# Kernel tuning notes

Measured on AMD Instinct MI355X. Metric: run time of the kernel, lower is better.

Reference implementation:

```python
import jax, jax.numpy as jnp
import numpy as np

H = 768       # hidden_size
HEADS = 8     # num_heads
T = 3         # num_timesteps
B = 128       # molecules in batch
N_ATOM = 48   # atoms per molecule
E_INTRA = 96  # intra-molecule directed edges per molecule
NPG = N_ATOM + 1          # nodes per graph (incl. virtual)
EPG = E_INTRA + N_ATOM    # edges per graph (incl. atom->virtual)
N = B * NPG
E = B * EPG


def setup_inputs() -> dict:
    key = jax.random.key(0)
    ks = jax.random.split(key, 10)
    atom_feat = jax.random.normal(ks[0], (B, N_ATOM, H), dtype=jnp.float32)
    mol_feat = jax.random.normal(ks[1], (B, H), dtype=jnp.float32)
    # node features with virtual node (=mol_feat) appended per graph, as in add_virtual_nodes_and_edges
    h_nodes = jnp.concatenate([atom_feat, mol_feat[:, None, :]], axis=1).reshape(N, H)
    off = jnp.arange(B, dtype=jnp.int32) * NPG
    intra_src = jax.random.randint(ks[2], (B, E_INTRA), 0, N_ATOM, dtype=jnp.int32) + off[:, None]
    intra_dst = jax.random.randint(ks[3], (B, E_INTRA), 0, N_ATOM, dtype=jnp.int32) + off[:, None]
    virt_src = jnp.arange(N_ATOM, dtype=jnp.int32)[None, :] + off[:, None]
    virt_dst = jnp.broadcast_to((off + N_ATOM)[:, None], (B, N_ATOM))
    src = jnp.concatenate([intra_src, virt_src], axis=1).reshape(E)
    dst = jnp.concatenate([intra_dst, virt_dst], axis=1).reshape(E)
    virtual_nids = off + N_ATOM  # last node of each graph (cumsum(batch_num_nodes)-1)
    attn_eids = ((jnp.arange(B, dtype=jnp.int32) * EPG)[:, None]
                 + E_INTRA + jnp.arange(N_ATOM, dtype=jnp.int32)[None, :]).reshape(-1)
    s = 0.02
    W_src = jax.random.normal(ks[4], (T, H, HEADS * H), dtype=jnp.float32) * s
    W_dst = jax.random.normal(ks[5], (T, H, HEADS * H), dtype=jnp.float32) * s
    attn_a = jax.random.normal(ks[6], (T, HEADS, H), dtype=jnp.float32) * s
    W_ih = jax.random.normal(ks[7], (T, 3 * H, H), dtype=jnp.float32) * s
    W_hh = jax.random.normal(ks[8], (T, 3 * H, H), dtype=jnp.float32) * s
    b_src = jnp.zeros((T, HEADS * H), jnp.float32)
    b_dst = jnp.zeros((T, HEADS * H), jnp.float32)
    b_ih = jnp.zeros((T, 3 * H), jnp.float32)
    b_hh = jnp.zeros((T, 3 * H), jnp.float32)
    return {"h_nodes": h_nodes, "mol_feat": mol_feat, "W_src": W_src, "b_src": b_src,
            "W_dst": W_dst, "b_dst": b_dst, "attn_a": attn_a, "W_ih": W_ih, "W_hh": W_hh,
            "b_ih": b_ih, "b_hh": b_hh, "src": src, "dst": dst,
            "virtual_nids": virtual_nids, "attn_eids": attn_eids}


def _gru_cell(x, hprev, W_ih_t, W_hh_t, b_ih_t, b_hh_t):
    # torch.nn.GRUCell: gates ordered r, z, n
    gi = x @ W_ih_t.T + b_ih_t
    gh = hprev @ W_hh_t.T + b_hh_t
    ir, iz, inn = jnp.split(gi, 3, axis=-1)
    hr, hz, hn = jnp.split(gh, 3, axis=-1)
    r = jax.nn.sigmoid(ir + hr)
    z = jax.nn.sigmoid(iz + hz)
    n = jnp.tanh(inn + r * hn)
    return (1.0 - z) * n + z * hprev


def _forward(h_nodes, mol_feat, W_src, b_src, W_dst, b_dst, attn_a,
             W_ih, W_hh, b_ih, b_hh, src, dst, virtual_nids, attn_eids):
    h = h_nodes
    mol_emb = mol_feat
    attns = []
    for t in range(T):
        # GATv2Conv (DGL, eval mode so feat_drop/attn_drop are identity)
        fs = (h @ W_src[t] + b_src[t]).reshape(N, HEADS, H)
        fd = (h @ W_dst[t] + b_dst[t]).reshape(N, HEADS, H)
        e = jax.nn.leaky_relu(fs[src] + fd[dst], negative_slope=0.2)  # [E, heads, H]
        logits = jnp.einsum('ehd,hd->eh', e, attn_a[t])               # [E, heads]
        # edge softmax over incoming edges per destination node
        m = jax.ops.segment_max(logits, dst, num_segments=N)
        ex = jnp.exp(logits - m[dst])
        ssum = jax.ops.segment_sum(ex, dst, num_segments=N)
        a = ex / ssum[dst]                                            # [E, heads]
        rst = jax.ops.segment_sum(a[:, :, None] * fs[src], dst, num_segments=N)  # [N, heads, H]
        h = rst.mean(axis=1)                                          # mean over heads
        out_virtual = h[virtual_nids]                                 # [B, H]
        mol_emb = jax.nn.relu(_gru_cell(out_virtual, mol_emb, W_ih[t], W_hh[t], b_ih[t], b_hh[t]))
        attns.append(a.mean(axis=1)[attn_eids])                       # attention on virtual edges
    return mol_emb, jnp.stack(attns)


def reference(h_nodes, mol_feat, W_src, b_src, W_dst, b_dst, attn_a,
              W_ih, W_hh, b_ih, b_hh, src, dst, virtual_nids, attn_eids):
    return _forward(h_nodes, mol_feat, W_src, b_src, W_dst, b_dst, attn_a,
                    W_ih, W_hh, b_ih, b_hh, src, dst, virtual_nids, attn_eids)
```

## Files before the change

### kernel.cpp

```cpp
#include <hip/hip_runtime.h>
#include <hip/hip_bf16.h>

typedef __hip_bfloat16 bf16;
typedef float f32x4 __attribute__((ext_vector_type(4)));
typedef __bf16 bf16x8 __attribute__((ext_vector_type(8)));
typedef short s16x8 __attribute__((ext_vector_type(8)));
typedef short s16x2 __attribute__((ext_vector_type(2)));

#define HDIM 768
#define NHEAD 8
#define BMOL 128
#define NPG 49
#define EPG 144
#define NNODE (BMOL * NPG)
#define NEDGE (BMOL * EPG)
#define NH 6144
#define G3 2304

__device__ __forceinline__ float b2f(short s) {
    unsigned int u = ((unsigned int)(unsigned short)s) << 16;
    return __builtin_bit_cast(float, u);
}

__device__ __forceinline__ void async16(const bf16* g, bf16* l) {
    __builtin_amdgcn_global_load_lds(
        (const __attribute__((address_space(1))) void*)g,
        (__attribute__((address_space(3))) void*)l, 16, 0, 0);
}

#define VMCNT(n) asm volatile("s_waitcnt vmcnt(" #n ")" ::: "memory")
#define SBAR()                                 \
    do {                                       \
        asm volatile("" ::: "memory");         \
        __builtin_amdgcn_s_barrier();          \
        asm volatile("" ::: "memory");         \
    } while (0)

__global__ __launch_bounds__(512, 2) void gemm_bt8(
    const bf16* __restrict__ A, const bf16* __restrict__ Bt0,
    const bf16* __restrict__ Bt1, const float* __restrict__ bias0,
    const float* __restrict__ bias1, bf16* __restrict__ C0,
    bf16* __restrict__ C1) {
    __shared__ __align__(16) char smem[131072];
    bf16* lA = (bf16*)smem;
    bf16* lB = (bf16*)(smem + 65536);

    const int tid = threadIdx.x;
    const int lane = tid & 63;
    const int wave = tid >> 6;
    const int l16 = lane & 15;
    const int quad = lane >> 4;
    const int wm = wave >> 2;
    const int wn = wave & 3;
    const int K = HDIM;

    int id = blockIdx.y * 24 + blockIdx.x;
    const int xcd = id & 7;
    const int loc = id >> 3;
    const int mc = loc / 15;
    const int rem = loc % 15;
    const int ncol = rem / 5;
    const int moff = rem % 5;
    const int m0 = (mc * 5 + moff) * 256;
    const int n0 = (xcd * 3 + ncol) * 256;

    const bf16* Bt = blockIdx.z ? Bt1 : Bt0;
    const float* bias = blockIdx.z ? bias1 : bias0;
    bf16* C = blockIdx.z ? C1 : C0;

    const int srow = tid >> 3;
    const int ecol =
        ((tid & 7) * 8) ^ ((srow & 1) * 32) ^ ((srow & 2) * 8);
    const bf16* gAr[4];
#pragma unroll
    for (int hc = 0; hc < 4; ++hc) {
        int r = m0 + srow + hc * 64;
        if (r > NNODE - 1) r = NNODE - 1;
        gAr[hc] = A + (size_t)r * K + ecol;
    }
    const bf16* gB = Bt + (size_t)(n0 + srow) * K + ecol;
    const size_t hstep = (size_t)128 * K;
    const size_t cstep = (size_t)64 * K;
    bf16* dA = lA + tid * 8;
    bf16* dB = lB + tid * 8;

#define STAGE_A(buf, h, kt)                                     \
    do {                                                        \
        bf16* _d = dA + (buf)*16384 + (h)*8192;                 \
        async16(gAr[(h)*2] + (size_t)(kt) * 64, _d);            \
        async16(gAr[(h)*2 + 1] + (size_t)(kt) * 64, _d + 4096); \
    } while (0)
#define STAGE_B(buf, h, kt)                                     \
    do {                                                        \
        const bf16* _s = gB + (h)*hstep + (size_t)(kt) * 64;    \
        bf16* _d = dB + (buf)*16384 + (h)*8192;                 \
        async16(_s, _d);                                        \
        async16(_s + cstep, _d + 4096);                         \
    } while (0)

    const int q16 = quad * 16;
    const int sw = ((l16 & 1) << 6) | ((l16 & 2) << 4);
    const char* laRow = (const char*)lA + wm * 16384 + l16 * 128;
    const char* lbRow =
        (const char*)lB + (wn >> 1) * 16384 + (wn & 1) * 8192 + l16 * 128;

#define LDA8(buf, f, ks) \
    (*(const bf16x8*)(laRow + (buf)*32768 + (f)*2048 + ((q16 + (ks)*64) ^ sw)))
#define LDB8(buf, j, ks) \
    (*(const bf16x8*)(lbRow + (buf)*32768 + (j)*2048 + ((q16 + (ks)*64) ^ sw)))

    f32x4 acc[8][4];
#pragma unroll
    for (int i = 0; i < 8; ++i)
#pragma unroll
        for (int j = 0; j < 4; ++j) acc[i][j] = (f32x4){0.f, 0.f, 0.f, 0.f};
    bf16x8 bfr[4][2];

#define MF(i, j, ks, areg)                                             \
    acc[i][j] = __builtin_amdgcn_mfma_f32_16x16x32_bf16(areg, bfr[j][ks], \
                                                        acc[i][j], 0, 0, 0)

#define PHASE(buf, q, LB, STG, WAIT)                                   \
    do {                                                               \
        bf16x8 a00 = LDA8(buf, (q)*2, 0);                              \
        bf16x8 a01 = LDA8(buf, (q)*2, 1);                              \
        bf16x8 a10 = LDA8(buf, (q)*2 + 1, 0);                          \
        bf16x8 a11 = LDA8(buf, (q)*2 + 1, 1);                          \
        if (LB) {                                                      \
            bfr[0][0] = LDB8(buf, 0, 0); bfr[0][1] = LDB8(buf, 0, 1);  \
            bfr[1][0] = LDB8(buf, 1, 0); bfr[1][1] = LDB8(buf, 1, 1);  \
            bfr[2][0] = LDB8(buf, 2, 0); bfr[2][1] = LDB8(buf, 2, 1);  \
            bfr[3][0] = LDB8(buf, 3, 0); bfr[3][1] = LDB8(buf, 3, 1);  \
        }                                                              \
        STG;                                                           \
        SBAR();                                                        \
        __builtin_amdgcn_s_setprio(1);                                 \
        MF((q)*2, 0, 0, a00); MF((q)*2, 1, 0, a00);                    \
        MF((q)*2, 2, 0, a00); MF((q)*2, 3, 0, a00);                    \
        MF((q)*2 + 1, 0, 0, a10); MF((q)*2 + 1, 1, 0, a10);            \
        MF((q)*2 + 1, 2, 0, a10); MF((q)*2 + 1, 3, 0, a10);            \
        MF((q)*2, 0, 1, a01); MF((q)*2, 1, 1, a01);                    \
        MF((q)*2, 2, 1, a01); MF((q)*2, 3, 1, a01);                    \
        MF((q)*2 + 1, 0, 1, a11); MF((q)*2 + 1, 1, 1, a11);            \
        MF((q)*2 + 1, 2, 1, a11); MF((q)*2 + 1, 3, 1, a11);            \
        __builtin_amdgcn_s_setprio(0);                                 \
        WAIT;                                                          \
        SBAR();                                                        \
    } while (0)

    STAGE_A(0, 0, 0); STAGE_A(0, 1, 0);
    STAGE_B(0, 0, 0); STAGE_B(0, 1, 0);
    STAGE_B(1, 0, 1); STAGE_B(1, 1, 1);
    VMCNT(4);
    SBAR();

    int t0 = 0;
    for (int it = 0; it < 5; ++it, t0 += 2) {
        PHASE(0, 0, 1, STAGE_A(1, 0, t0 + 1), );
        PHASE(0, 1, 0, STAGE_A(1, 1, t0 + 1), );
        PHASE(0, 2, 0, STAGE_B(0, 0, t0 + 2), );
        PHASE(0, 3, 0, STAGE_B(0, 1, t0 + 2), VMCNT(4));
        PHASE(1, 0, 1, STAGE_A(0, 0, t0 + 2), );
        PHASE(1, 1, 0, STAGE_A(0, 1, t0 + 2), );
        PHASE(1, 2, 0, STAGE_B(1, 0, t0 + 3), );
        PHASE(1, 3, 0, STAGE_B(1, 1, t0 + 3), VMCNT(4));
    }
    PHASE(0, 0, 1, STAGE_A(1, 0, 11), );
    PHASE(0, 1, 0, STAGE_A(1, 1, 11), );
    PHASE(0, 2, 0, , );
    PHASE(0, 3, 0, , VMCNT(0));
    PHASE(1, 0, 1, , );
    PHASE(1, 1, 0, , );
    PHASE(1, 2, 0, , );
    PHASE(1, 3, 0, , );

    __syncthreads();
#pragma unroll
    for (int i = 0; i < 8; ++i) {
        const int rloc = wm * 128 + i * 16 + quad * 4;
#pragma unroll
        for (int j = 0; j < 4; ++j) {
            const int cloc = wn * 64 + j * 16 + l16;
            const float bc = bias[n0 + cloc];
#pragma unroll
            for (int r = 0; r < 4; ++r) {
                const int rr = rloc + r;
                int off = (rr * 512 + cloc * 2) ^ ((rr & 4) ? 32 : 0);
                *(bf16*)(smem + off) = __float2bfloat16(acc[i][j][r] + bc);
            }
        }
    }
    __syncthreads();
#pragma unroll
    for (int k = 0; k < 16; ++k) {
        const int off = (k * 512 + tid) * 16;
        const int row = off >> 9;
        const int bcol = (off & 511) ^ ((row & 4) ? 32 : 0);
        if (m0 + row < NNODE) {
            bf16x8 v = *(const bf16x8*)(smem + off);
            *(bf16x8*)(C + (size_t)(m0 + row) * NH + n0 + (bcol >> 1)) = v;
        }
    }
#undef PHASE
#undef MF
#undef LDA8
#undef LDB8
#undef STAGE_A
#undef STAGE_B
}

__global__ __launch_bounds__(256) void gemm_small(
    const bf16* __restrict__ hws, const int* __restrict__ vnids,
    const bf16* __restrict__ A1, const bf16* __restrict__ B0,
    const bf16* __restrict__ B1, const float* __restrict__ bias0,
    const float* __restrict__ bias1, float* __restrict__ C0,
    float* __restrict__ C1, const bf16* __restrict__ A0) {
    __shared__ __align__(16) bf16 lA[32 * 32];
    __shared__ __align__(16) bf16 lB[256 * 32];
    const int tid = threadIdx.x;
    const int lane = tid & 63;
    const int wave = tid >> 6;
    const int l16 = lane & 15;
    const int quad = lane >> 4;
    const int K = HDIM;
    const int y0 = blockIdx.y * 32;
    const int x0 = blockIdx.x * 256;
    const bf16* Bt = blockIdx.z ? B1 : B0;
    const float* bias = blockIdx.z ? bias1 : bias0;
    float* C = blockIdx.z ? C1 : C0;

    const int ry = y0 + (tid >> 2);
    const bf16* gA;
    if (blockIdx.z)
        gA = A1 + (size_t)ry * K + (tid & 3) * 8;
    else if (A0)
        gA = A0 + (size_t)(ry & 127) * K + (tid & 3) * 8;
    else
        gA = hws + (size_t)vnids[ry & 127] * K + (tid & 3) * 8;
    const bf16* gB = Bt + (size_t)(x0 + (tid >> 2)) * K + (tid & 3) * 8;
    bf16* lAp = lA + tid * 8;
    bf16* lBp = lB + tid * 8;
    const size_t rstep = (size_t)64 * K;

    f32x4 acc[2][4];
#pragma unroll
    for (int i = 0; i < 2; ++i)
#pragma unroll
        for (int j = 0; j < 4; ++j) acc[i][j] = (f32x4){0.f, 0.f, 0.f, 0.f};

    for (int k0 = 0; k0 < K; k0 += 32) {
        __syncthreads();
        if (tid < 128) async16(gA + k0, lAp);
        async16(gB + k0, lBp);
        async16(gB + k0 + rstep, lBp + 2048);
        async16(gB + k0 + 2 * rstep, lBp + 4096);
        async16(gB + k0 + 3 * rstep, lBp + 6144);
        __syncthreads();
        bf16x8 af[2], bfr[4];
#pragma unroll
        for (int i = 0; i < 2; ++i)
            af[i] = *(const bf16x8*)(lA + (i * 16 + l16) * 32 + quad * 8);
#pragma unroll
        for (int j = 0; j < 4; ++j)
            bfr[j] = *(const bf16x8*)(lB + (wave * 64 + j * 16 + l16) * 32 +
                                      quad * 8);
#pragma unroll
        for (int i = 0; i < 2; ++i)
#pragma unroll
            for (int j = 0; j < 4; ++j)
                acc[i][j] = __builtin_amdgcn_mfma_f32_16x16x32_bf16(
                    af[i], bfr[j], acc[i][j], 0, 0, 0);
    }

#pragma unroll
    for (int i = 0; i < 2; ++i) {
#pragma unroll
        for (int j = 0; j < 4; ++j) {
            int row = y0 + i * 16 + quad * 4;
            int col = x0 + wave * 64 + j * 16 + l16;
            float bc = bias[col];
#pragma unroll
            for (int r = 0; r < 4; ++r)
                C[(size_t)(row + r) * G3 + col] = acc[i][j][r] + bc;
        }
    }
}

__global__ __launch_bounds__(256) void gemm_gather_bt(
    const bf16* __restrict__ hws, const int* __restrict__ vnids,
    const bf16* __restrict__ Bt, const float* __restrict__ bias,
    bf16* __restrict__ C) {
    __shared__ __align__(16) bf16 lA[32 * 32];
    __shared__ __align__(16) bf16 lB[256 * 32];
    const int tid = threadIdx.x;
    const int lane = tid & 63;
    const int wave = tid >> 6;
    const int l16 = lane & 15;
    const int quad = lane >> 4;
    const int K = HDIM;
    const int y0 = blockIdx.y * 32;
    const int x0 = blockIdx.x * 256;

    const int ry = y0 + (tid >> 2);
    const bf16* gA = hws + (size_t)vnids[ry & 127] * K + (tid & 3) * 8;
    const bf16* gB = Bt + (size_t)(x0 + (tid >> 2)) * K + (tid & 3) * 8;
    bf16* lAp = lA + tid * 8;
    bf16* lBp = lB + tid * 8;
    const size_t rstep = (size_t)64 * K;

    f32x4 acc[2][4];
#pragma unroll
    for (int i = 0; i < 2; ++i)
#pragma unroll
        for (int j = 0; j < 4; ++j) acc[i][j] = (f32x4){0.f, 0.f, 0.f, 0.f};

    for (int k0 = 0; k0 < K; k0 += 32) {
        __syncthreads();
        if (tid < 128) async16(gA + k0, lAp);
        async16(gB + k0, lBp);
        async16(gB + k0 + rstep, lBp + 2048);
        async16(gB + k0 + 2 * rstep, lBp + 4096);
        async16(gB + k0 + 3 * rstep, lBp + 6144);
        __syncthreads();
        bf16x8 af[2], bfr[4];
#pragma unroll
        for (int i = 0; i < 2; ++i)
            af[i] = *(const bf16x8*)(lA + (i * 16 + l16) * 32 + quad * 8);
#pragma unroll
        for (int j = 0; j < 4; ++j)
            bfr[j] = *(const bf16x8*)(lB + (wave * 64 + j * 16 + l16) * 32 +
                                      quad * 8);
#pragma unroll
        for (int i = 0; i < 2; ++i)
#pragma unroll
            for (int j = 0; j < 4; ++j)
                acc[i][j] = __builtin_amdgcn_mfma_f32_16x16x32_bf16(
                    af[i], bfr[j], acc[i][j], 0, 0, 0);
    }

#pragma unroll
    for (int i = 0; i < 2; ++i) {
#pragma unroll
        for (int j = 0; j < 4; ++j) {
            int row = y0 + i * 16 + quad * 4;
            int col = x0 + wave * 64 + j * 16 + l16;
            float bc = bias[col];
#pragma unroll
            for (int r = 0; r < 4; ++r)
                C[(size_t)(row + r) * NH + col] =
                    __float2bfloat16(acc[i][j][r] + bc);
        }
    }
}

__global__ __launch_bounds__(256) void transpose_w(
    const float* __restrict__ W, bf16* __restrict__ Wt, int K, int Nn) {
    __shared__ bf16 tile[64][65];
    const int z = blockIdx.z;
    const float* Wp = W + (size_t)z * K * Nn;
    bf16* Wtp = Wt + (size_t)z * K * Nn;
    const int n0 = blockIdx.x * 64;
    const int k0 = blockIdx.y * 64;
    const int tx = threadIdx.x & 63;
    const int ty = threadIdx.x >> 6;
#pragma unroll
    for (int i = 0; i < 64; i += 4)
        tile[ty + i][tx] = __float2bfloat16(Wp[(size_t)(k0 + ty + i) * Nn + n0 + tx]);
    __syncthreads();
#pragma unroll
    for (int i = 0; i < 64; i += 4)
        Wtp[(size_t)(n0 + ty + i) * K + k0 + tx] = tile[tx][ty + i];
}

__global__ void cvt_kernel(const float* __restrict__ x, bf16* __restrict__ y,
                           int n) {
    int i = blockIdx.x * 256 + threadIdx.x;
    if (i < n) y[i] = __float2bfloat16(x[i]);
}

__global__ __launch_bounds__(256) void logits_kernel(
    const bf16* __restrict__ fs, const bf16* __restrict__ fd,
    const float* __restrict__ attn_a_t, const int* __restrict__ src,
    const int* __restrict__ dst, float* __restrict__ logits) {
    __shared__ __align__(16) float s_a[NH];
    const int tid = threadIdx.x;
    for (int p = tid; p < NH; p += 256) s_a[p] = attn_a_t[p];
    __syncthreads();

    const int wave = tid >> 6;
    const int lane = tid & 63;
    const int e = blockIdx.x * 4 + wave;
    const int gs = src[e], gd = dst[e];
    const bf16* ps = fs + (size_t)gs * NH;
    const bf16* pd = fd + (size_t)gd * NH;
    const int h = lane >> 3;
    const int s = lane & 7;
    const int base = h * HDIM + s * 8;

    float acc = 0.f;
#pragma unroll
    for (int j = 0; j < 12; ++j) {
        const int off = base + j * 64;
        s16x8 a8 = *(const s16x8*)(ps + off);
        s16x8 d8 = *(const s16x8*)(pd + off);
        f32x4 av0 = *(const f32x4*)(s_a + off);
        f32x4 av1 = *(const f32x4*)(s_a + off + 4);
#pragma unroll
        for (int u = 0; u < 4; ++u) {
            float x = b2f(a8[u]) + b2f(d8[u]);
            x = (x > 0.f) ? x : 0.2f * x;
            acc += x * av0[u];
        }
#pragma unroll
        for (int u = 0; u < 4; ++u) {
            float x = b2f(a8[4 + u]) + b2f(d8[4 + u]);
            x = (x > 0.f) ? x : 0.2f * x;
            acc += x * av1[u];
        }
    }
    acc += __shfl_xor(acc, 1);
    acc += __shfl_xor(acc, 2);
    acc += __shfl_xor(acc, 4);
    if (s == 0) logits[(size_t)e * NHEAD + h] = acc;
}

__global__ __launch_bounds__(256) void logits_virt_kernel(
    const bf16* __restrict__ fs, const bf16* __restrict__ fdv,
    const float* __restrict__ attn_a_t, float* __restrict__ lgv) {
    __shared__ __align__(16) float s_a[NH];
    const int tid = threadIdx.x;
    for (int p = tid; p < NH; p += 256) s_a[p] = attn_a_t[p];
    __syncthreads();

    const int wave = tid >> 6;
    const int lane = tid & 63;
    const int e = blockIdx.x * 4 + wave;
    const int b = e / 48;
    const int i = e - b * 48;
    const bf16* ps = fs + (size_t)(b * NPG + i) * NH;
    const bf16* pd = fdv + (size_t)b * NH;
    const int h = lane >> 3;
    const int s = lane & 7;
    const int base = h * HDIM + s * 8;

    float acc = 0.f;
#pragma unroll
    for (int j = 0; j < 12; ++j) {
        const int off = base + j * 64;
        s16x8 a8 = *(const s16x8*)(ps + off);
        s16x8 d8 = *(const s16x8*)(pd + off);
        f32x4 av0 = *(const f32x4*)(s_a + off);
        f32x4 av1 = *(const f32x4*)(s_a + off + 4);
#pragma unroll
        for (int u = 0; u < 4; ++u) {
            float x = b2f(a8[u]) + b2f(d8[u]);
            x = (x > 0.f) ? x : 0.2f * x;
            acc += x * av0[u];
        }
#pragma unroll
        for (int u = 0; u < 4; ++u) {
            float x = b2f(a8[4 + u]) + b2f(d8[4 + u]);
            x = (x > 0.f) ? x : 0.2f * x;
            acc += x * av1[u];
        }
    }
    acc += __shfl_xor(acc, 1);
    acc += __shfl_xor(acc, 2);
    acc += __shfl_xor(acc, 4);
    if (s == 0) lgv[(size_t)e * NHEAD + h] = acc;
}

__global__ __launch_bounds__(256) void softmax_kernel(
    const float* __restrict__ logits, const int* __restrict__ dst,
    float* __restrict__ w, float* __restrict__ outv) {
    __shared__ float s_logit[EPG * NHEAD];
    __shared__ float s_w[EPG * NHEAD];
    __shared__ int s_ld[EPG];
    __shared__ float s_m[NPG * NHEAD], s_inv[NPG * NHEAD];
    const int tid = threadIdx.x;
    const int b = blockIdx.x;
    for (int p = tid; p < EPG * NHEAD; p += 256)
        s_logit[p] = logits[(size_t)b * EPG * NHEAD + p];
    if (tid < EPG) s_ld[tid] = dst[b * EPG + tid] - b * NPG;
    __syncthreads();

    for (int p = tid; p < NPG * NHEAD; p += 256) {
        int n = p >> 3, h = p & 7;
        float m = -3.0e38f;
        for (int le = 0; le < EPG; ++le)
            if (s_ld[le] == n) m = fmaxf(m, s_logit[le * NHEAD + h]);
        float ss = 0.f;
        for (int le = 0; le < EPG; ++le)
            if (s_ld[le] == n) ss += __expf(s_logit[le * NHEAD + h] - m);
        s_m[p] = m;
        s_inv[p] = (ss > 0.f) ? 1.f / ss : 0.f;
    }
    __syncthreads();

    for (int p = tid; p < EPG * NHEAD; p += 256) {
        int le = p >> 3, h = p & 7;
        int ld = s_ld[le];
        float a =
            0.125f * __expf(s_logit[p] - s_m[ld * NHEAD + h]) * s_inv[ld * NHEAD + h];
        s_w[p] = a;
        w[(size_t)b * EPG * NHEAD + p] = a;
    }
    __syncthreads();
    if (tid < 48) {
        float s = 0.f;
#pragma unroll
        for (int h = 0; h < NHEAD; ++h) s += s_w[(96 + tid) * NHEAD + h];
        outv[b * 48 + tid] = s;
    }
}

__global__ __launch_bounds__(64) void softmax_virt_kernel(
    const float* __restrict__ lgv, float* __restrict__ wv,
    float* __restrict__ outv) {
    __shared__ float s_w[48 * NHEAD];
    const int b = blockIdx.x;
    const int tid = threadIdx.x;
    if (tid < NHEAD) {
        const int h = tid;
        float m = -3.0e38f;
        for (int i = 0; i < 48; ++i)
            m = fmaxf(m, lgv[(size_t)(b * 48 + i) * NHEAD + h]);
        float ss = 0.f;
        for (int i = 0; i < 48; ++i)
            ss += __expf(lgv[(size_t)(b * 48 + i) * NHEAD + h] - m);
        float inv = (ss > 0.f) ? 1.f / ss : 0.f;
        for (int i = 0; i < 48; ++i) {
            float a =
                0.125f * __expf(lgv[(size_t)(b * 48 + i) * NHEAD + h] - m) * inv;
            s_w[i * NHEAD + h] = a;
            wv[(size_t)(b * 48 + i) * NHEAD + h] = a;
        }
    }
    __syncthreads();
    if (tid < 48) {
        float s = 0.f;
#pragma unroll
        for (int h = 0; h < NHEAD; ++h) s += s_w[tid * NHEAD + h];
        outv[b * 48 + tid] = s;
    }
}

__global__ __launch_bounds__(256) void aggregate_kernel(
    const bf16* __restrict__ fs, const float* __restrict__ w,
    const int* __restrict__ src, const int* __restrict__ dst,
    bf16* __restrict__ hout) {
    __shared__ float acc[NPG * 128];
    __shared__ float s_w[EPG * NHEAD];
    __shared__ int s_gs[EPG], s_ld[EPG];
    const int tid = threadIdx.x;
    const int c = blockIdx.x;
    const int b = blockIdx.y;
    const int grp = tid >> 6;
    const int l = tid & 63;
    if (tid < EPG) {
        int e = b * EPG + tid;
        s_gs[tid] = src[e];
        s_ld[tid] = dst[e] - b * NPG;
    }
    for (int p = tid; p < EPG * NHEAD; p += 256)
        s_w[p] = w[(size_t)b * EPG * NHEAD + p];
    for (int p = tid; p < NPG * 128; p += 256) acc[p] = 0.f;
    __syncthreads();

    const int dim = c * 128 + l * 2;
    for (int le4 = 0; le4 < EPG; le4 += 4) {
        const int le = le4 + grp;
        const bf16* p = fs + (size_t)s_gs[le] * NH + dim;
        float sum0 = 0.f, sum1 = 0.f;
#pragma unroll
        for (int h = 0; h < NHEAD; ++h) {
            s16x2 v = *(const s16x2*)(p + h * HDIM);
            float wv = s_w[le * NHEAD + h];
            sum0 += wv * b2f(v[0]);
            sum1 += wv * b2f(v[1]);
        }
        float* ap = &acc[s_ld[le] * 128 + l * 2];
        atomicAdd(ap, sum0);
        atomicAdd(ap + 1, sum1);
    }
    __syncthreads();
    for (int p = tid; p < NPG * 128; p += 256) {
        int n = p >> 7, d = p & 127;
        hout[((size_t)b * NPG + n) * HDIM + c * 128 + d] =
            __float2bfloat16(acc[p]);
    }
}

__global__ __launch_bounds__(256) void aggregate_virt_kernel(
    const bf16* __restrict__ fs, const float* __restrict__ wv,
    bf16* __restrict__ hv) {
    __shared__ float acc[128];
    __shared__ float s_w[48 * NHEAD];
    const int tid = threadIdx.x;
    const int c = blockIdx.x;
    const int b = blockIdx.y;
    const int grp = tid >> 6;
    const int l = tid & 63;
    for (int p = tid; p < 48 * NHEAD; p += 256)
        s_w[p] = wv[(size_t)b * 48 * NHEAD + p];
    if (tid < 128) acc[tid] = 0.f;
    __syncthreads();

    const int dim = c * 128 + l * 2;
    float sum0 = 0.f, sum1 = 0.f;
    for (int le = grp; le < 48; le += 4) {
        const bf16* p = fs + (size_t)(b * NPG + le) * NH + dim;
#pragma unroll
        for (int h = 0; h < NHEAD; ++h) {
            s16x2 v = *(const s16x2*)(p + h * HDIM);
            float w_ = s_w[le * NHEAD + h];
            sum0 += w_ * b2f(v[0]);
            sum1 += w_ * b2f(v[1]);
        }
    }
    atomicAdd(&acc[l * 2], sum0);
    atomicAdd(&acc[l * 2 + 1], sum1);
    __syncthreads();
    if (tid < 128)
        hv[(size_t)b * HDIM + c * 128 + tid] = __float2bfloat16(acc[tid]);
}

__global__ void init_memb_kernel(const float* __restrict__ mf,
                                 float* __restrict__ m32,
                                 bf16* __restrict__ m16) {
    int idx = blockIdx.x * 256 + threadIdx.x;
    float f = mf[idx];
    m32[idx] = f;
    m16[idx] = __float2bfloat16(f);
}

__global__ void gru_gate_kernel(const float* __restrict__ gi,
                                const float* __restrict__ gh,
                                float* __restrict__ m32, bf16* __restrict__ m16,
                                float* __restrict__ outp, int last) {
    int idx = blockIdx.x * 256 + threadIdx.x;
    int b = idx / HDIM, d = idx - b * HDIM;
    const float* gib = gi + (size_t)b * G3;
    const float* ghb = gh + (size_t)b * G3;
    float ir = gib[d], iz = gib[HDIM + d], in_ = gib[2 * HDIM + d];
    float hr = ghb[d], hz = ghb[HDIM + d], hn = ghb[2 * HDIM + d];
    float r = 1.f / (1.f + __expf(-(ir + hr)));
    float z = 1.f / (1.f + __expf(-(iz + hz)));
    float n = tanhf(in_ + r * hn);
    float hprev = m32[idx];
    float hnew = (1.f - z) * n + z * hprev;
    hnew = fmaxf(hnew, 0.f);
    m32[idx] = hnew;
    m16[idx] = __float2bfloat16(hnew);
    if (last) outp[idx] = hnew;
}

extern "C" void kernel_launch(void* const* d_in, const int* in_sizes, int n_in,
                              void* d_out, int out_size, void* d_ws,
                              size_t ws_size, hipStream_t stream) {
    const float* h_nodes = (const float*)d_in[0];
    const float* mol_feat = (const float*)d_in[1];
    const float* W_src = (const float*)d_in[2];
    const float* b_src = (const float*)d_in[3];
    const float* W_dst = (const float*)d_in[4];
    const float* b_dst = (const float*)d_in[5];
    const float* attn_a = (const float*)d_in[6];
    const float* W_ih = (const float*)d_in[7];
    const float* W_hh = (const float*)d_in[8];
    const float* b_ih = (const float*)d_in[9];
    const float* b_hh = (const float*)d_in[10];
    const int* src = (const int*)d_in[11];
    const int* dst = (const int*)d_in[12];
    const int* vnids = (const int*)d_in[13];
    float* out = (float*)d_out;

    char* p = (char*)d_ws;
    auto alloc = [&](size_t bytes) {
        char* r = p;
        p += (bytes + 255) & ~(size_t)255;
        return r;
    };
    bf16* wsrcT = (bf16*)alloc((size_t)3 * NH * HDIM * 2);
    bf16* wdstT = (bf16*)alloc((size_t)3 * NH * HDIM * 2);
    bf16* wihB = (bf16*)alloc((size_t)3 * G3 * HDIM * 2);
    bf16* whhB = (bf16*)alloc((size_t)3 * G3 * HDIM * 2);
    bf16* fs = (bf16*)alloc((size_t)NNODE * NH * 2);
    bf16* fd = (bf16*)alloc((size_t)NNODE * NH * 2);
    bf16* h_ws = (bf16*)alloc((size_t)NNODE * HDIM * 2);
    float* lg = (float*)alloc((size_t)NEDGE * NHEAD * 4);
    float* w_e = (float*)alloc((size_t)NEDGE * NHEAD * 4);
    float* memb32 = (float*)alloc((size_t)BMOL * HDIM * 4);
    bf16* memb16 = (bf16*)alloc((size_t)BMOL * HDIM * 2);
    float* gi = (float*)alloc((size_t)BMOL * G3 * 4);
    float* gh = (float*)alloc((size_t)BMOL * G3 * 4);

    dim3 tgrid(NH / 64, HDIM / 64, 3);
    transpose_w<<<tgrid, 256, 0, stream>>>(W_src, wsrcT, HDIM, NH);
    transpose_w<<<tgrid, 256, 0, stream>>>(W_dst, wdstT, HDIM, NH);
    {
        int n = 3 * G3 * HDIM;
        cvt_kernel<<<(n + 255) / 256, 256, 0, stream>>>(W_ih, wihB, n);
        cvt_kernel<<<(n + 255) / 256, 256, 0, stream>>>(W_hh, whhB, n);
    }
    {
        int n = NNODE * HDIM;
        cvt_kernel<<<(n + 255) / 256, 256, 0, stream>>>(h_nodes, h_ws, n);
    }
    init_memb_kernel<<<BMOL * HDIM / 256, 256, 0, stream>>>(mol_feat, memb32,
                                                            memb16);

    for (int t = 0; t < 3; ++t) {
        if (t < 2) {
            gemm_bt8<<<dim3(24, 25, 2), 512, 0, stream>>>(
                h_ws, wsrcT + (size_t)t * NH * HDIM,
                wdstT + (size_t)t * NH * HDIM, b_src + (size_t)t * NH,
                b_dst + (size_t)t * NH, fs, fd);
            logits_kernel<<<NEDGE / 4, 256, 0, stream>>>(
                fs, fd, attn_a + (size_t)t * NHEAD * HDIM, src, dst, lg);
            softmax_kernel<<<BMOL, 256, 0, stream>>>(
                lg, dst, w_e, out + BMOL * HDIM + t * BMOL * 48);
            aggregate_kernel<<<dim3(6, BMOL), 256, 0, stream>>>(fs, w_e, src,
                                                                dst, h_ws);
            gemm_small<<<dim3(G3 / 256, 4, 2), 256, 0, stream>>>(
                h_ws, vnids, memb16, wihB + (size_t)t * G3 * HDIM,
                whhB + (size_t)t * G3 * HDIM, b_ih + (size_t)t * G3,
                b_hh + (size_t)t * G3, gi, gh, (const bf16*)nullptr);
            gru_gate_kernel<<<BMOL * HDIM / 256, 256, 0, stream>>>(
                gi, gh, memb32, memb16, out, 0);
        } else {
            gemm_bt8<<<dim3(24, 25, 1), 512, 0, stream>>>(
                h_ws, wsrcT + (size_t)t * NH * HDIM,
                wdstT + (size_t)t * NH * HDIM, b_src + (size_t)t * NH,
                b_dst + (size_t)t * NH, fs, fd);
            gemm_gather_bt<<<dim3(NH / 256, 4), 256, 0, stream>>>(
                h_ws, vnids, wdstT + (size_t)t * NH * HDIM,
                b_dst + (size_t)t * NH, fd);
            logits_virt_kernel<<<(BMOL * 48) / 4, 256, 0, stream>>>(
                fs, fd, attn_a + (size_t)t * NHEAD * HDIM, lg);
            softmax_virt_kernel<<<BMOL, 64, 0, stream>>>(
                lg, w_e, out + BMOL * HDIM + t * BMOL * 48);
            aggregate_virt_kernel<<<dim3(6, BMOL), 256, 0, stream>>>(
                fs, w_e, h_ws);
            gemm_small<<<dim3(G3 / 256, 4, 2), 256, 0, stream>>>(
                h_ws, vnids, memb16, wihB + (size_t)t * G3 * HDIM,
                whhB + (size_t)t * G3 * HDIM, b_ih + (size_t)t * G3,
                b_hh + (size_t)t * G3, gi, gh, h_ws);
            gru_gate_kernel<<<BMOL * HDIM / 256, 256, 0, stream>>>(
                gi, gh, memb32, memb16, out, 1);
        }
    }
}
```

Measured before the change: 1.045 ms.

## Merge setup conversion kernels, fuse virtual logits+softmax, widen aggregate and logits work per block

Combines the two weight transposes into one launch and the four fp32-to-bf16 conversion kernels into a single cvt_all kernel. For the last timestep, virtual-edge logits and softmax are fused into one per-molecule kernel that keeps logits in shared memory. Each logits block now handles 16 edges instead of 4, and each aggregate block covers 256 dims using 4-wide loads instead of 128 dims with 2-wide loads. Together these cut launch count and global round trips, at the cost of fewer blocks (less parallelism) in logits, aggregate and virtual attention.

```diff
diff --git a/kernel.cpp b/kernel.cpp
--- a/kernel.cpp
+++ b/kernel.cpp
@@ -5,7 +5,7 @@
 typedef float f32x4 __attribute__((ext_vector_type(4)));
 typedef __bf16 bf16x8 __attribute__((ext_vector_type(8)));
 typedef short s16x8 __attribute__((ext_vector_type(8)));
-typedef short s16x2 __attribute__((ext_vector_type(2)));
+typedef short s16x4 __attribute__((ext_vector_type(4)));
 
 #define HDIM 768
 #define NHEAD 8
@@ -353,12 +353,15 @@
     }
 }
 
-__global__ __launch_bounds__(256) void transpose_w(
-    const float* __restrict__ W, bf16* __restrict__ Wt, int K, int Nn) {
+__global__ __launch_bounds__(256) void transpose_w2(
+    const float* __restrict__ Wa, bf16* __restrict__ WaT,
+    const float* __restrict__ Wb, bf16* __restrict__ WbT, int K, int Nn) {
     __shared__ bf16 tile[64][65];
     const int z = blockIdx.z;
-    const float* Wp = W + (size_t)z * K * Nn;
-    bf16* Wtp = Wt + (size_t)z * K * Nn;
+    const float* Wp = (z < 3 ? Wa + (size_t)z * K * Nn
+                             : Wb + (size_t)(z - 3) * K * Nn);
+    bf16* Wtp = (z < 3 ? WaT + (size_t)z * K * Nn
+                       : WbT + (size_t)(z - 3) * K * Nn);
     const int n0 = blockIdx.x * 64;
     const int k0 = blockIdx.y * 64;
     const int tx = threadIdx.x & 63;
@@ -372,10 +375,31 @@
         Wtp[(size_t)(n0 + ty + i) * K + k0 + tx] = tile[tx][ty + i];
 }
 
-__global__ void cvt_kernel(const float* __restrict__ x, bf16* __restrict__ y,
-                           int n) {
+__global__ void cvt_all(const float* __restrict__ W_ih,
+                        const float* __restrict__ W_hh, bf16* __restrict__ wihB,
+                        bf16* __restrict__ whhB,
+                        const float* __restrict__ h_nodes,
+                        bf16* __restrict__ h_ws, const float* __restrict__ mf,
+                        float* __restrict__ m32, bf16* __restrict__ m16) {
+    const int N1 = 3 * G3 * HDIM;
+    const int N2 = N1 + 3 * G3 * HDIM;
+    const int N3 = N2 + NNODE * HDIM;
+    const int N4 = N3 + BMOL * HDIM;
     int i = blockIdx.x * 256 + threadIdx.x;
-    if (i < n) y[i] = __float2bfloat16(x[i]);
+    if (i < N1) {
+        wihB[i] = __float2bfloat16(W_ih[i]);
+    } else if (i < N2) {
+        int k = i - N1;
+        whhB[k] = __float2bfloat16(W_hh[k]);
+    } else if (i < N3) {
+        int k = i - N2;
+        h_ws[k] = __float2bfloat16(h_nodes[k]);
+    } else if (i < N4) {
+        int k = i - N3;
+        float f = mf[k];
+        m32[k] = f;
+        m16[k] = __float2bfloat16(f);
+    }
 }
 
 __global__ __launch_bounds__(256) void logits_kernel(
@@ -389,85 +413,44 @@
 
     const int wave = tid >> 6;
     const int lane = tid & 63;
-    const int e = blockIdx.x * 4 + wave;
-    const int gs = src[e], gd = dst[e];
-    const bf16* ps = fs + (size_t)gs * NH;
-    const bf16* pd = fd + (size_t)gd * NH;
     const int h = lane >> 3;
     const int s = lane & 7;
     const int base = h * HDIM + s * 8;
-
-    float acc = 0.f;
-#pragma unroll
-    for (int j = 0; j < 12; ++j) {
-        const int off = base + j * 64;
-        s16x8 a8 = *(const s16x8*)(ps + off);
-        s16x8 d8 = *(const s16x8*)(pd + off);
-        f32x4 av0 = *(const f32x4*)(s_a + off);
-        f32x4 av1 = *(const f32x4*)(s_a + off + 4);
-#pragma unroll
-        for (int u = 0; u < 4; ++u) {
-            float x = b2f(a8[u]) + b2f(d8[u]);
-            x = (x > 0.f) ? x : 0.2f * x;
-            acc += x * av0[u];
-        }
-#pragma unroll
-        for (int u = 0; u < 4; ++u) {
-            float x = b2f(a8[4 + u]) + b2f(d8[4 + u]);
-            x = (x > 0.f) ? x : 0.2f * x;
-            acc += x * av1[u];
-        }
-    }
-    acc += __shfl_xor(acc, 1);
-    acc += __shfl_xor(acc, 2);
-    acc += __shfl_xor(acc, 4);
-    if (s == 0) logits[(size_t)e * NHEAD + h] = acc;
-}
-
-__global__ __launch_bounds__(256) void logits_virt_kernel(
-    const bf16* __restrict__ fs, const bf16* __restrict__ fdv,
-    const float* __restrict__ attn_a_t, float* __restrict__ lgv) {
-    __shared__ __align__(16) float s_a[NH];
-    const int tid = threadIdx.x;
-    for (int p = tid; p < NH; p += 256) s_a[p] = attn_a_t[p];
-    __syncthreads();
-
-    const int wave = tid >> 6;
-    const int lane = tid & 63;
-    const int e = blockIdx.x * 4 + wave;
-    const int b = e / 48;
-    const int i = e - b * 48;
-    const bf16* ps = fs + (size_t)(b * NPG + i) * NH;
-    const bf16* pd = fdv + (size_t)b * NH;
-    const int h = lane >> 3;
-    const int s = lane & 7;
-    const int base = h * HDIM + s * 8;
-
-    float acc = 0.f;
-#pragma unroll
-    for (int j = 0; j < 12; ++j) {
-        const int off = base + j * 64;
-        s16x8 a8 = *(const s16x8*)(ps + off);
-        s16x8 d8 = *(const s16x8*)(pd + off);
-        f32x4 av0 = *(const f32x4*)(s_a + off);
-        f32x4 av1 = *(const f32x4*)(s_a + off + 4);
-#pragma unroll
-        for (int u = 0; u < 4; ++u) {
-            float x = b2f(a8[u]) + b2f(d8[u]);
-            x = (x > 0.f) ? x : 0.2f * x;
-            acc += x * av0[u];
-        }
-#pragma unroll
-        for (int u = 0; u < 4; ++u) {
-            float x = b2f(a8[4 + u]) + b2f(d8[4 + u]);
-            x = (x > 0.f) ? x : 0.2f * x;
-            acc += x * av1[u];
-        }
-    }
-    acc += __shfl_xor(acc, 1);
-    acc += __shfl_xor(acc, 2);
-    acc += __shfl_xor(acc, 4);
-    if (s == 0) lgv[(size_t)e * NHEAD + h] = acc;
+    const int e0 = blockIdx.x * 16 + wave * 4;
+
+#pragma unroll
+    for (int ee = 0; ee < 4; ++ee) {
+        const int e = e0 + ee;
+        const int gs = src[e], gd = dst[e];
+        const bf16* ps = fs + (size_t)gs * NH;
+        const bf16* pd = fd + (size_t)gd * NH;
+
+        float acc = 0.f;
+#pragma unroll
+        for (int j = 0; j < 12; ++j) {
+            const int off = base + j * 64;
+            s16x8 a8 = *(const s16x8*)(ps + off);
+            s16x8 d8 = *(const s16x8*)(pd + off);
+            f32x4 av0 = *(const f32x4*)(s_a + off);
+            f32x4 av1 = *(const f32x4*)(s_a + off + 4);
+#pragma unroll
+            for (int u = 0; u < 4; ++u) {
+                float x = b2f(a8[u]) + b2f(d8[u]);
+                x = (x > 0.f) ? x : 0.2f * x;
+                acc += x * av0[u];
+            }
+#pragma unroll
+            for (int u = 0; u < 4; ++u) {
+                float x = b2f(a8[4 + u]) + b2f(d8[4 + u]);
+                x = (x > 0.f) ? x : 0.2f * x;
+                acc += x * av1[u];
+            }
+        }
+        acc += __shfl_xor(acc, 1);
+        acc += __shfl_xor(acc, 2);
+        acc += __shfl_xor(acc, 4);
+        if (s == 0) logits[(size_t)e * NHEAD + h] = acc;
+    }
 }
 
 __global__ __launch_bounds__(256) void softmax_kernel(
@@ -514,34 +497,74 @@
     }
 }
 
-__global__ __launch_bounds__(64) void softmax_virt_kernel(
-    const float* __restrict__ lgv, float* __restrict__ wv,
+__global__ __launch_bounds__(256) void attn_virt_kernel(
+    const bf16* __restrict__ fs, const bf16* __restrict__ fdv,
+    const float* __restrict__ attn_a_t, float* __restrict__ wv,
     float* __restrict__ outv) {
+    __shared__ __align__(16) float s_a[NH];
+    __shared__ float s_lg[48 * NHEAD];
     __shared__ float s_w[48 * NHEAD];
+    const int tid = threadIdx.x;
     const int b = blockIdx.x;
-    const int tid = threadIdx.x;
+    for (int p = tid; p < NH; p += 256) s_a[p] = attn_a_t[p];
+    __syncthreads();
+
+    const int wave = tid >> 6;
+    const int lane = tid & 63;
+    const int h = lane >> 3;
+    const int s = lane & 7;
+    const int base = h * HDIM + s * 8;
+    const bf16* pd = fdv + (size_t)b * NH;
+
+    for (int i = wave; i < 48; i += 4) {
+        const bf16* ps = fs + (size_t)(b * NPG + i) * NH;
+        float acc = 0.f;
+#pragma unroll
+        for (int j = 0; j < 12; ++j) {
+            const int off = base + j * 64;
+            s16x8 a8 = *(const s16x8*)(ps + off);
+            s16x8 d8 = *(const s16x8*)(pd + off);
+            f32x4 av0 = *(const f32x4*)(s_a + off);
+            f32x4 av1 = *(const f32x4*)(s_a + off + 4);
+#pragma unroll
+            for (int u = 0; u < 4; ++u) {
+                float x = b2f(a8[u]) + b2f(d8[u]);
+                x = (x > 0.f) ? x : 0.2f * x;
+                acc += x * av0[u];
+            }
+#pragma unroll
+            for (int u = 0; u < 4; ++u) {
+                float x = b2f(a8[4 + u]) + b2f(d8[4 + u]);
+                x = (x > 0.f) ? x : 0.2f * x;
+                acc += x * av1[u];
+            }
+        }
+        acc += __shfl_xor(acc, 1);
+        acc += __shfl_xor(acc, 2);
+        acc += __shfl_xor(acc, 4);
+        if (s == 0) s_lg[i * NHEAD + h] = acc;
+    }
+    __syncthreads();
+
     if (tid < NHEAD) {
-        const int h = tid;
+        const int h2 = tid;
         float m = -3.0e38f;
-        for (int i = 0; i < 48; ++i)
-            m = fmaxf(m, lgv[(size_t)(b * 48 + i) * NHEAD + h]);
+        for (int i = 0; i < 48; ++i) m = fmaxf(m, s_lg[i * NHEAD + h2]);
         float ss = 0.f;
-        for (int i = 0; i < 48; ++i)
-            ss += __expf(lgv[(size_t)(b * 48 + i) * NHEAD + h] - m);
+        for (int i = 0; i < 48; ++i) ss += __expf(s_lg[i * NHEAD + h2] - m);
         float inv = (ss > 0.f) ? 1.f / ss : 0.f;
         for (int i = 0; i < 48; ++i) {
-            float a =
-                0.125f * __expf(lgv[(size_t)(b * 48 + i) * NHEAD + h] - m) * inv;
-            s_w[i * NHEAD + h] = a;
-            wv[(size_t)(b * 48 + i) * NHEAD + h] = a;
+            float a = 0.125f * __expf(s_lg[i * NHEAD + h2] - m) * inv;
+            s_w[i * NHEAD + h2] = a;
+            wv[(size_t)(b * 48 + i) * NHEAD + h2] = a;
         }
     }
     __syncthreads();
     if (tid < 48) {
-        float s = 0.f;
-#pragma unroll
-        for (int h = 0; h < NHEAD; ++h) s += s_w[tid * NHEAD + h];
-        outv[b * 48 + tid] = s;
+        float sum = 0.f;
+#pragma unroll
+        for (int hh = 0; hh < NHEAD; ++hh) sum += s_w[tid * NHEAD + hh];
+        outv[b * 48 + tid] = sum;
     }
 }
 
@@ -549,7 +572,7 @@
     const bf16* __restrict__ fs, const float* __restrict__ w,
     const int* __restrict__ src, const int* __restrict__ dst,
     bf16* __restrict__ hout) {
-    __shared__ float acc[NPG * 128];
+    __shared__ float acc[NPG * 256];
     __shared__ float s_w[EPG * NHEAD];
     __shared__ int s_gs[EPG], s_ld[EPG];
     const int tid = threadIdx.x;
@@ -564,29 +587,33 @@
     }
     for (int p = tid; p < EPG * NHEAD; p += 256)
         s_w[p] = w[(size_t)b * EPG * NHEAD + p];
-    for (int p = tid; p < NPG * 128; p += 256) acc[p] = 0.f;
-    __syncthreads();
-
-    const int dim = c * 128 + l * 2;
+    for (int p = tid; p < NPG * 256; p += 256) acc[p] = 0.f;
+    __syncthreads();
+
+    const int dim = c * 256 + l * 4;
     for (int le4 = 0; le4 < EPG; le4 += 4) {
         const int le = le4 + grp;
         const bf16* p = fs + (size_t)s_gs[le] * NH + dim;
-        float sum0 = 0.f, sum1 = 0.f;
+        float s0 = 0.f, s1 = 0.f, s2 = 0.f, s3 = 0.f;
 #pragma unroll
         for (int h = 0; h < NHEAD; ++h) {
-            s16x2 v = *(const s16x2*)(p + h * HDIM);
+            s16x4 v = *(const s16x4*)(p + h * HDIM);
             float wv = s_w[le * NHEAD + h];
-            sum0 += wv * b2f(v[0]);
-            sum1 += wv * b2f(v[1]);
-        }
-        float* ap = &acc[s_ld[le] * 128 + l * 2];
-        atomicAdd(ap, sum0);
-        atomicAdd(ap + 1, sum1);
-    }
-    __syncthreads();
-    for (int p = tid; p < NPG * 128; p += 256) {
-        int n = p >> 7, d = p & 127;
-        hout[((size_t)b * NPG + n) * HDIM + c * 128 + d] =
+            s0 += wv * b2f(v[0]);
+            s1 += wv * b2f(v[1]);
+            s2 += wv * b2f(v[2]);
+            s3 += wv * b2f(v[3]);
+        }
+        float* ap = &acc[s_ld[le] * 256 + l * 4];
+        atomicAdd(ap, s0);
+        atomicAdd(ap + 1, s1);
+        atomicAdd(ap + 2, s2);
+        atomicAdd(ap + 3, s3);
+    }
+    __syncthreads();
+    for (int p = tid; p < NPG * 256; p += 256) {
+        int n = p >> 8, d = p & 255;
+        hout[((size_t)b * NPG + n) * HDIM + c * 256 + d] =
             __float2bfloat16(acc[p]);
     }
 }
@@ -612,10 +639,10 @@
         const bf16* p = fs + (size_t)(b * NPG + le) * NH + dim;
 #pragma unroll
         for (int h = 0; h < NHEAD; ++h) {
-            s16x2 v = *(const s16x2*)(p + h * HDIM);
+            short2 v = *(const short2*)(p + h * HDIM);
             float w_ = s_w[le * NHEAD + h];
-            sum0 += w_ * b2f(v[0]);
-            sum1 += w_ * b2f(v[1]);
+            sum0 += w_ * b2f(v.x);
+            sum1 += w_ * b2f(v.y);
         }
     }
     atomicAdd(&acc[l * 2], sum0);
@@ -623,15 +650,6 @@
     __syncthreads();
     if (tid < 128)
         hv[(size_t)b * HDIM + c * 128 + tid] = __float2bfloat16(acc[tid]);
-}
-
-__global__ void init_memb_kernel(const float* __restrict__ mf,
-                                 float* __restrict__ m32,
-                                 bf16* __restrict__ m16) {
-    int idx = blockIdx.x * 256 + threadIdx.x;
-    float f = mf[idx];
-    m32[idx] = f;
-    m16[idx] = __float2bfloat16(f);
 }
 
 __global__ void gru_gate_kernel(const float* __restrict__ gi,
@@ -694,20 +712,13 @@
     float* gi = (float*)alloc((size_t)BMOL * G3 * 4);
     float* gh = (float*)alloc((size_t)BMOL * G3 * 4);
 
-    dim3 tgrid(NH / 64, HDIM / 64, 3);
-    transpose_w<<<tgrid, 256, 0, stream>>>(W_src, wsrcT, HDIM, NH);
-    transpose_w<<<tgrid, 256, 0, stream>>>(W_dst, wdstT, HDIM, NH);
+    transpose_w2<<<dim3(NH / 64, HDIM / 64, 6), 256, 0, stream>>>(
+        W_src, wsrcT, W_dst, wdstT, HDIM, NH);
     {
-        int n = 3 * G3 * HDIM;
-        cvt_kernel<<<(n + 255) / 256, 256, 0, stream>>>(W_ih, wihB, n);
-        cvt_kernel<<<(n + 255) / 256, 256, 0, stream>>>(W_hh, whhB, n);
-    }
-    {
-        int n = NNODE * HDIM;
-        cvt_kernel<<<(n + 255) / 256, 256, 0, stream>>>(h_nodes, h_ws, n);
-    }
-    init_memb_kernel<<<BMOL * HDIM / 256, 256, 0, stream>>>(mol_feat, memb32,
-                                                            memb16);
+        int ntot = 2 * 3 * G3 * HDIM + NNODE * HDIM + BMOL * HDIM;
+        cvt_all<<<(ntot + 255) / 256, 256, 0, stream>>>(
+            W_ih, W_hh, wihB, whhB, h_nodes, h_ws, mol_feat, memb32, memb16);
+    }
 
     for (int t = 0; t < 3; ++t) {
         if (t < 2) {
@@ -715,11 +726,11 @@
                 h_ws, wsrcT + (size_t)t * NH * HDIM,
                 wdstT + (size_t)t * NH * HDIM, b_src + (size_t)t * NH,
                 b_dst + (size_t)t * NH, fs, fd);
-            logits_kernel<<<NEDGE / 4, 256, 0, stream>>>(
+            logits_kernel<<<NEDGE / 16, 256, 0, stream>>>(
                 fs, fd, attn_a + (size_t)t * NHEAD * HDIM, src, dst, lg);
             softmax_kernel<<<BMOL, 256, 0, stream>>>(
                 lg, dst, w_e, out + BMOL * HDIM + t * BMOL * 48);
-            aggregate_kernel<<<dim3(6, BMOL), 256, 0, stream>>>(fs, w_e, src,
+            aggregate_kernel<<<dim3(3, BMOL), 256, 0, stream>>>(fs, w_e, src,
                                                                 dst, h_ws);
             gemm_small<<<dim3(G3 / 256, 4, 2), 256, 0, stream>>>(
                 h_ws, vnids, memb16, wihB + (size_t)t * G3 * HDIM,
@@ -735,10 +746,9 @@
             gemm_gather_bt<<<dim3(NH / 256, 4), 256, 0, stream>>>(
                 h_ws, vnids, wdstT + (size_t)t * NH * HDIM,
                 b_dst + (size_t)t * NH, fd);
-            logits_virt_kernel<<<(BMOL * 48) / 4, 256, 0, stream>>>(
-                fs, fd, attn_a + (size_t)t * NHEAD * HDIM, lg);
-            softmax_virt_kernel<<<BMOL, 64, 0, stream>>>(
-                lg, w_e, out + BMOL * HDIM + t * BMOL * 48);
+            attn_virt_kernel<<<BMOL, 256, 0, stream>>>(
+                fs, fd, attn_a + (size_t)t * NHEAD * HDIM, w_e,
+                out + BMOL * HDIM + t * BMOL * 48);
             aggregate_virt_kernel<<<dim3(6, BMOL), 256, 0, stream>>>(
                 fs, w_e, h_ws);
             gemm_small<<<dim3(G3 / 256, 4, 2), 256, 0, stream>>>(
```

New measurement: 1.107 ms. 1.06x slower.
